# Optimization experiments

Measured on AMD Instinct MI355X. Metric: run time of the kernel, lower is better.

The kernel has to match this reference:

```python
import jax, jax.numpy as jnp
import numpy as np

N_NODES = 100000
N_EDGES = 1600000
D_IN = 64
D_HID = 128
BN_EPS = 1e-5


def setup_inputs() -> dict:
    key = jax.random.key(0)
    ks = jax.random.split(key, 8)
    x = jax.random.normal(ks[0], (N_NODES, D_IN), dtype=jnp.float32)
    edge_index = jax.random.randint(ks[1], (2, N_EDGES), 0, N_NODES, dtype=jnp.int64)
    # MLP params (Linear stores W as [out, in]; we keep [in, out] for x @ W)
    s1 = 1.0 / np.sqrt(D_IN)
    s2 = 1.0 / np.sqrt(D_HID)
    W1 = jax.random.uniform(ks[2], (D_IN, D_HID), minval=-s1, maxval=s1, dtype=jnp.float32)
    b1 = jax.random.uniform(ks[3], (D_HID,), minval=-s1, maxval=s1, dtype=jnp.float32)
    W2 = jax.random.uniform(ks[4], (D_HID, D_HID), minval=-s2, maxval=s2, dtype=jnp.float32)
    b2 = jax.random.uniform(ks[5], (D_HID,), minval=-s2, maxval=s2, dtype=jnp.float32)
    gamma = jnp.ones((D_HID,), dtype=jnp.float32)
    beta = jnp.zeros((D_HID,), dtype=jnp.float32)
    return {"x": x, "edge_index": edge_index, "W1": W1, "b1": b1,
            "W2": W2, "b2": b2, "gamma": gamma, "beta": beta}


def reference(x, edge_index, W1, b1, W2, b2, gamma, beta):
    src, dst = edge_index[0], edge_index[1]
    # GIN sum aggregation: agg[i] = sum_{(j->i) in E} x[j]
    agg = jax.ops.segment_sum(x[src], dst, num_segments=N_NODES)
    h = x + agg  # eps = 0 (GINConv default)
    # 2-layer MLP with ReLU
    h = jax.nn.relu(h @ W1 + b1)
    h = h @ W2 + b2
    # outer ReLU
    h = jax.nn.relu(h)
    # BatchNorm1d (training mode: biased batch statistics over nodes)
    mean = jnp.mean(h, axis=0)
    var = jnp.var(h, axis=0)
    h = (h - mean) * jax.lax.rsqrt(var + BN_EPS) * gamma + beta
    return h
```

## Files before the change

### kernel.cpp

```cpp
#include <hip/hip_runtime.h>

#define N_NODES 100000
#define N_EDGES 1600000
#define D_IN 64
#define D_HID 128

typedef __attribute__((ext_vector_type(8))) _Float16 half8;
typedef __attribute__((ext_vector_type(4))) float f32x4;

__global__ __launch_bounds__(256) void k_hist(const int* __restrict__ dst,
                                              int* __restrict__ counts) {
    int e = blockIdx.x * 256 + threadIdx.x;
    atomicAdd(&counts[dst[e]], 1);
}

__global__ __launch_bounds__(256) void k_scan1(const int* __restrict__ counts,
                                               int* __restrict__ loc,
                                               int* __restrict__ bsum) {
    __shared__ int tmp[256];
    int t = threadIdx.x;
    int base = blockIdx.x * 1024 + t * 4;
    int v0 = (base + 0 < N_NODES) ? counts[base + 0] : 0;
    int v1 = (base + 1 < N_NODES) ? counts[base + 1] : 0;
    int v2 = (base + 2 < N_NODES) ? counts[base + 2] : 0;
    int v3 = (base + 3 < N_NODES) ? counts[base + 3] : 0;
    tmp[t] = v0 + v1 + v2 + v3;
    __syncthreads();
    for (int off = 1; off < 256; off <<= 1) {
        int val = tmp[t];
        int add = (t >= off) ? tmp[t - off] : 0;
        __syncthreads();
        tmp[t] = val + add;
        __syncthreads();
    }
    int excl = t ? tmp[t - 1] : 0;
    if (base + 0 < N_NODES) loc[base + 0] = excl;
    if (base + 1 < N_NODES) loc[base + 1] = excl + v0;
    if (base + 2 < N_NODES) loc[base + 2] = excl + v0 + v1;
    if (base + 3 < N_NODES) loc[base + 3] = excl + v0 + v1 + v2;
    if (t == 255) bsum[blockIdx.x] = tmp[255];
}

__global__ void k_scan2(const int* __restrict__ bsum, int* __restrict__ bpref) {
    __shared__ int tmp[128];
    int t = threadIdx.x;
    tmp[t] = (t < 98) ? bsum[t] : 0;
    __syncthreads();
    for (int off = 1; off < 128; off <<= 1) {
        int val = tmp[t];
        int add = (t >= off) ? tmp[t - off] : 0;
        __syncthreads();
        tmp[t] = val + add;
        __syncthreads();
    }
    bpref[t] = t ? tmp[t - 1] : 0;
}

__global__ __launch_bounds__(256) void k_scan3(const int* __restrict__ loc,
                                               const int* __restrict__ bpref,
                                               int* __restrict__ offs) {
    int i = blockIdx.x * 256 + threadIdx.x;
    if (i < N_NODES) offs[i] = loc[i] + bpref[i >> 10];
}

__global__ __launch_bounds__(256) void k_fill(const int* __restrict__ src,
                                              const int* __restrict__ dst,
                                              int* __restrict__ offs,
                                              int* __restrict__ srcs) {
    int e = blockIdx.x * 256 + threadIdx.x;
    int p = atomicAdd(&offs[dst[e]], 1);
    srcs[p] = src[e];
}

__global__ __launch_bounds__(256) void k_gather(const float* __restrict__ x,
                                                const int* __restrict__ offs_end,
                                                const int* __restrict__ counts,
                                                const int* __restrict__ srcs,
                                                _Float16* __restrict__ aggh) {
    int wid = (blockIdx.x * 256 + threadIdx.x) >> 6;
    int lane = threadIdx.x & 63;
    int end = offs_end[wid];
    int beg = end - counts[wid];
    float sum = x[(size_t)wid * 64 + lane];
    int e = beg;
    for (; e + 4 <= end; e += 4) {
        int s0 = srcs[e], s1 = srcs[e + 1], s2 = srcs[e + 2], s3 = srcs[e + 3];
        float a0 = x[(size_t)s0 * 64 + lane];
        float a1 = x[(size_t)s1 * 64 + lane];
        float a2 = x[(size_t)s2 * 64 + lane];
        float a3 = x[(size_t)s3 * 64 + lane];
        sum += a0 + a1 + a2 + a3;
    }
    for (; e < end; ++e) sum += x[(size_t)srcs[e] * 64 + lane];
    aggh[(size_t)wid * 64 + lane] = (_Float16)sum;
}

__global__ __launch_bounds__(256) void k_pack(const float* __restrict__ W1,
                                              const float* __restrict__ W2,
                                              _Float16* __restrict__ W1p,
                                              _Float16* __restrict__ W2p) {
    int t = blockIdx.x * 256 + threadIdx.x;
    if (t < 1024) {
        int l = t & 63;
        int row = ((t >> 9) & 1) * 32 + (l >> 4) * 8;
        int col = ((t >> 6) & 7) * 16 + (l & 15);
#pragma unroll
        for (int i = 0; i < 8; ++i)
            W1p[t * 8 + i] = (_Float16)W1[(row + i) * 128 + col];
    } else {
        int s = t - 1024;
        int l = s & 63;
        int row = (s >> 9) * 32 + (l >> 4) * 8;
        int col = ((s >> 6) & 7) * 16 + (l & 15);
#pragma unroll
        for (int i = 0; i < 8; ++i)
            W2p[s * 8 + i] = (_Float16)W2[(row + i) * 128 + col];
    }
}

__global__ __launch_bounds__(256) void k_gemm1(const _Float16* __restrict__ A,
                                               const _Float16* __restrict__ Wp,
                                               const float* __restrict__ bias,
                                               _Float16* __restrict__ H) {
    int lane = threadIdx.x & 63, wv = threadIdx.x >> 6;
    int row0 = blockIdx.x * 64 + wv * 16;
    int ar = row0 + (lane & 15);
    if (ar > N_NODES - 1) ar = N_NODES - 1;
    int ac = (lane >> 4) * 8;
    half8 a0 = *(const half8*)&A[(size_t)ar * 64 + ac];
    half8 a1 = *(const half8*)&A[(size_t)ar * 64 + 32 + ac];
    f32x4 acc[8];
#pragma unroll
    for (int ct = 0; ct < 8; ++ct) {
        half8 w0 = *(const half8*)&Wp[(size_t)(ct * 64 + lane) * 8];
        half8 w1 = *(const half8*)&Wp[(size_t)(512 + ct * 64 + lane) * 8];
        f32x4 c = {0.f, 0.f, 0.f, 0.f};
        c = __builtin_amdgcn_mfma_f32_16x16x32_f16(a0, w0, c, 0, 0, 0);
        c = __builtin_amdgcn_mfma_f32_16x16x32_f16(a1, w1, c, 0, 0, 0);
        acc[ct] = c;
    }
    int g = lane >> 4, cl = lane & 15;
#pragma unroll
    for (int ct = 0; ct < 8; ++ct) {
        int col = ct * 16 + cl;
        float b = bias[col];
#pragma unroll
        for (int r = 0; r < 4; ++r) {
            int row = row0 + g * 4 + r;
            if (row < N_NODES) {
                float v = fmaxf(acc[ct][r] + b, 0.f);
                H[(size_t)row * 128 + col] = (_Float16)v;
            }
        }
    }
}

__global__ __launch_bounds__(256) void k_gemm2(const _Float16* __restrict__ A,
                                               const _Float16* __restrict__ Wp,
                                               const float* __restrict__ bias,
                                               float* __restrict__ OUT,
                                               float* __restrict__ stats) {
    __shared__ float sred[4][256];
    int lane = threadIdx.x & 63, wv = threadIdx.x >> 6;
    int row0 = blockIdx.x * 64 + wv * 16;
    int ar = row0 + (lane & 15);
    if (ar > N_NODES - 1) ar = N_NODES - 1;
    int ac = (lane >> 4) * 8;
    half8 a[4];
#pragma unroll
    for (int kt = 0; kt < 4; ++kt)
        a[kt] = *(const half8*)&A[(size_t)ar * 128 + kt * 32 + ac];
    int g = lane >> 4, cl = lane & 15;
#pragma unroll
    for (int ct = 0; ct < 8; ++ct) {
        f32x4 c = {0.f, 0.f, 0.f, 0.f};
#pragma unroll
        for (int kt = 0; kt < 4; ++kt) {
            half8 w = *(const half8*)&Wp[(size_t)((kt * 8 + ct) * 64 + lane) * 8];
            c = __builtin_amdgcn_mfma_f32_16x16x32_f16(a[kt], w, c, 0, 0, 0);
        }
        int col = ct * 16 + cl;
        float b = bias[col];
        float s = 0.f, q = 0.f;
#pragma unroll
        for (int r = 0; r < 4; ++r) {
            int row = row0 + g * 4 + r;
            float v = fmaxf(c[r] + b, 0.f);
            if (row < N_NODES) {
                OUT[(size_t)row * 128 + col] = v;
                s += v; q += v * v;
            }
        }
        s += __shfl_xor(s, 16); s += __shfl_xor(s, 32);
        q += __shfl_xor(q, 16); q += __shfl_xor(q, 32);
        if (g == 0) { sred[wv][col] = s; sred[wv][128 + col] = q; }
    }
    __syncthreads();
    int tid = threadIdx.x;
    float v = sred[0][tid] + sred[1][tid] + sred[2][tid] + sred[3][tid];
    unsafeAtomicAdd(&stats[tid], v);
}

__global__ void k_finalize(const float* __restrict__ stats,
                           const float* __restrict__ gamma,
                           const float* __restrict__ beta,
                           float* __restrict__ ss) {
    int c = threadIdx.x;
    float mean = stats[c] * (1.0f / N_NODES);
    float var = stats[128 + c] * (1.0f / N_NODES) - mean * mean;
    float scale = gamma[c] * rsqrtf(var + 1e-5f);
    ss[c] = scale;
    ss[128 + c] = beta[c] - mean * scale;
}

__global__ __launch_bounds__(256) void k_bn(float4* __restrict__ out,
                                            const float4* __restrict__ ss) {
    int stride = gridDim.x * 256;
    for (int f = blockIdx.x * 256 + threadIdx.x; f < N_NODES * 32; f += stride) {
        int c4 = f & 31;
        float4 sc = ss[c4];
        float4 sh = ss[32 + c4];
        float4 v = out[f];
        v.x = v.x * sc.x + sh.x;
        v.y = v.y * sc.y + sh.y;
        v.z = v.z * sc.z + sh.z;
        v.w = v.w * sc.w + sh.w;
        out[f] = v;
    }
}

extern "C" void kernel_launch(void* const* d_in, const int* in_sizes, int n_in,
                              void* d_out, int out_size, void* d_ws, size_t ws_size,
                              hipStream_t stream) {
    const float* x     = (const float*)d_in[0];
    const int*   ei    = (const int*)d_in[1];
    const float* W1    = (const float*)d_in[2];
    const float* b1    = (const float*)d_in[3];
    const float* W2    = (const float*)d_in[4];
    const float* b2    = (const float*)d_in[5];
    const float* gamma = (const float*)d_in[6];
    const float* beta  = (const float*)d_in[7];
    float* out = (float*)d_out;

    char* w = (char*)d_ws;
    _Float16* aggh = (_Float16*)w;  w += (size_t)N_NODES * D_IN * 2;
    _Float16* h1h  = (_Float16*)w;  w += (size_t)N_NODES * D_HID * 2;
    int* srcs      = (int*)w;       w += (size_t)N_EDGES * 4;
    int* counts    = (int*)w;       w += N_NODES * 4;
    int* loc       = (int*)w;       w += N_NODES * 4;
    int* offs      = (int*)w;       w += N_NODES * 4;
    int* bsum      = (int*)w;       w += 512;
    int* bpref     = (int*)w;       w += 512;
    float* stats   = (float*)w;     w += 1024;
    float* ss      = (float*)w;     w += 1024;
    _Float16* W1p  = (_Float16*)w;  w += 16384;
    _Float16* W2p  = (_Float16*)w;  w += 32768;

    const int* src = ei;
    const int* dst = ei + N_EDGES;

    (void)hipMemsetAsync(counts, 0, N_NODES * sizeof(int), stream);
    (void)hipMemsetAsync(stats, 0, 256 * sizeof(float), stream);

    k_pack <<<12, 256, 0, stream>>>(W1, W2, W1p, W2p);
    k_hist <<<N_EDGES / 256, 256, 0, stream>>>(dst, counts);
    k_scan1<<<98, 256, 0, stream>>>(counts, loc, bsum);
    k_scan2<<<1, 128, 0, stream>>>(bsum, bpref);
    k_scan3<<<(N_NODES + 255) / 256, 256, 0, stream>>>(loc, bpref, offs);
    k_fill <<<N_EDGES / 256, 256, 0, stream>>>(src, dst, offs, srcs);
    k_gather<<<N_NODES / 4, 256, 0, stream>>>(x, offs, counts, srcs, aggh);

    k_gemm1<<<(N_NODES + 63) / 64, 256, 0, stream>>>(aggh, W1p, b1, h1h);
    k_gemm2<<<(N_NODES + 63) / 64, 256, 0, stream>>>(h1h, W2p, b2, out, stats);
    k_finalize<<<1, 128, 0, stream>>>(stats, gamma, beta, ss);
    k_bn<<<2048, 256, 0, stream>>>((float4*)out, (const float4*)ss);
}
```

Before: 447.5 us.

## Replace atomic CSR build with two-level bucketed sort and fp16 gather

Builds the destination-sorted edge list with a two-pass radix-style partition: per-block bin histograms in shared memory, a single-block scan, a scatter into 512-node bins, then a per-bin counting sort staged through shared memory. This replaces global atomics on 100k counters and random scattered writes. Node features are pre-converted to fp16, and the gather reads half2 with two edges per wave half, which halves gather bandwidth at the cost of fp16 rounding of the inputs before summation. The offsets array now carries an end sentinel instead of counts.

Measured after the change: 383.5 us. 1.17x faster.

```diff
diff --git a/kernel.cpp b/kernel.cpp
--- a/kernel.cpp
+++ b/kernel.cpp
@@ -1,98 +1,169 @@
 #include <hip/hip_runtime.h>
+#include <hip/hip_fp16.h>
 
 #define N_NODES 100000
 #define N_EDGES 1600000
 #define D_IN 64
 #define D_HID 128
+#define NBINS 196
+#define NBLK 200
+#define EPB 8000
+#define FCAP 10240
 
 typedef __attribute__((ext_vector_type(8))) _Float16 half8;
 typedef __attribute__((ext_vector_type(4))) float f32x4;
 
-__global__ __launch_bounds__(256) void k_hist(const int* __restrict__ dst,
-                                              int* __restrict__ counts) {
-    int e = blockIdx.x * 256 + threadIdx.x;
-    atomicAdd(&counts[dst[e]], 1);
-}
-
-__global__ __launch_bounds__(256) void k_scan1(const int* __restrict__ counts,
-                                               int* __restrict__ loc,
-                                               int* __restrict__ bsum) {
-    __shared__ int tmp[256];
+__device__ inline float2 h2f(unsigned u) {
+    __half2 h = __builtin_bit_cast(__half2, u);
+    return __half22float2(h);
+}
+__device__ inline unsigned f2h(float a, float b) {
+    __half2 h = __floats2half2_rn(a, b);
+    return __builtin_bit_cast(unsigned, h);
+}
+
+__global__ __launch_bounds__(256) void k_xhalf(const float4* __restrict__ x4,
+                                               uint2* __restrict__ xh2) {
+    int i = blockIdx.x * 256 + threadIdx.x;
+    float4 v = x4[i];
+    uint2 o;
+    o.x = f2h(v.x, v.y);
+    o.y = f2h(v.z, v.w);
+    xh2[i] = o;
+}
+
+__global__ __launch_bounds__(256) void k_pcount(const int* __restrict__ dst,
+                                                int* __restrict__ pbh) {
+    __shared__ int hist[NBINS];
+    int t = threadIdx.x, b = blockIdx.x;
+    if (t < NBINS) hist[t] = 0;
+    __syncthreads();
+    for (int i = t; i < EPB; i += 256)
+        atomicAdd(&hist[dst[b * EPB + i] >> 9], 1);
+    __syncthreads();
+    if (t < NBINS) pbh[t * NBLK + b] = hist[t];
+}
+
+__global__ void k_pscan(const int* __restrict__ pbh, int* __restrict__ pbo,
+                        int* __restrict__ binstart, int* __restrict__ offs) {
+    __shared__ int part[256];
+    const int TOT = NBINS * NBLK;
     int t = threadIdx.x;
-    int base = blockIdx.x * 1024 + t * 4;
-    int v0 = (base + 0 < N_NODES) ? counts[base + 0] : 0;
-    int v1 = (base + 1 < N_NODES) ? counts[base + 1] : 0;
-    int v2 = (base + 2 < N_NODES) ? counts[base + 2] : 0;
-    int v3 = (base + 3 < N_NODES) ? counts[base + 3] : 0;
-    tmp[t] = v0 + v1 + v2 + v3;
+    int lo = t * 154, hi = lo + 154 < TOT ? lo + 154 : TOT;
+    int s = 0;
+    for (int i = lo; i < hi; ++i) s += pbh[i];
+    part[t] = s;
     __syncthreads();
     for (int off = 1; off < 256; off <<= 1) {
-        int val = tmp[t];
-        int add = (t >= off) ? tmp[t - off] : 0;
+        int val = part[t];
+        int add = (t >= off) ? part[t - off] : 0;
         __syncthreads();
-        tmp[t] = val + add;
+        part[t] = val + add;
         __syncthreads();
     }
-    int excl = t ? tmp[t - 1] : 0;
-    if (base + 0 < N_NODES) loc[base + 0] = excl;
-    if (base + 1 < N_NODES) loc[base + 1] = excl + v0;
-    if (base + 2 < N_NODES) loc[base + 2] = excl + v0 + v1;
-    if (base + 3 < N_NODES) loc[base + 3] = excl + v0 + v1 + v2;
-    if (t == 255) bsum[blockIdx.x] = tmp[255];
-}
-
-__global__ void k_scan2(const int* __restrict__ bsum, int* __restrict__ bpref) {
-    __shared__ int tmp[128];
-    int t = threadIdx.x;
-    tmp[t] = (t < 98) ? bsum[t] : 0;
-    __syncthreads();
-    for (int off = 1; off < 128; off <<= 1) {
-        int val = tmp[t];
-        int add = (t >= off) ? tmp[t - off] : 0;
+    int run = t ? part[t - 1] : 0;
+    for (int i = lo; i < hi; ++i) {
+        int v = pbh[i];
+        pbo[i] = run;
+        if ((i % NBLK) == 0) binstart[i / NBLK] = run;
+        run += v;
+    }
+    if (t == 0) { binstart[NBINS] = N_EDGES; offs[N_NODES] = N_EDGES; }
+}
+
+__global__ __launch_bounds__(256) void k_pscatter(const int* __restrict__ src,
+                                                  const int* __restrict__ dst,
+                                                  const int* __restrict__ pbo,
+                                                  unsigned* __restrict__ packed) {
+    __shared__ int cur[NBINS];
+    int t = threadIdx.x, b = blockIdx.x;
+    if (t < NBINS) cur[t] = pbo[t * NBLK + b];
+    __syncthreads();
+    for (int i = t; i < EPB; i += 256) {
+        int e = b * EPB + i;
+        int d = dst[e];
+        int bin = d >> 9;
+        int p = atomicAdd(&cur[bin], 1);
+        packed[p] = ((unsigned)(d & 511) << 17) | (unsigned)src[e];
+    }
+}
+
+__global__ __launch_bounds__(256) void k_fsort(const unsigned* __restrict__ packed,
+                                               const int* __restrict__ binstart,
+                                               int* __restrict__ offs,
+                                               int* __restrict__ srcs) {
+    __shared__ int nh[512];
+    __shared__ int cur[512];
+    __shared__ int part[256];
+    __shared__ int stage[FCAP];
+    int t = threadIdx.x, bin = blockIdx.x;
+    int base = binstart[bin];
+    int n = binstart[bin + 1] - base;
+    nh[t] = 0; nh[t + 256] = 0;
+    __syncthreads();
+    for (int i = t; i < n; i += 256)
+        atomicAdd(&nh[packed[base + i] >> 17], 1);
+    __syncthreads();
+    int a0 = nh[2 * t], a1 = nh[2 * t + 1];
+    part[t] = a0 + a1;
+    __syncthreads();
+    for (int off = 1; off < 256; off <<= 1) {
+        int val = part[t];
+        int add = (t >= off) ? part[t - off] : 0;
         __syncthreads();
-        tmp[t] = val + add;
+        part[t] = val + add;
         __syncthreads();
     }
-    bpref[t] = t ? tmp[t - 1] : 0;
-}
-
-__global__ __launch_bounds__(256) void k_scan3(const int* __restrict__ loc,
-                                               const int* __restrict__ bpref,
-                                               int* __restrict__ offs) {
-    int i = blockIdx.x * 256 + threadIdx.x;
-    if (i < N_NODES) offs[i] = loc[i] + bpref[i >> 10];
-}
-
-__global__ __launch_bounds__(256) void k_fill(const int* __restrict__ src,
-                                              const int* __restrict__ dst,
-                                              int* __restrict__ offs,
-                                              int* __restrict__ srcs) {
-    int e = blockIdx.x * 256 + threadIdx.x;
-    int p = atomicAdd(&offs[dst[e]], 1);
-    srcs[p] = src[e];
-}
-
-__global__ __launch_bounds__(256) void k_gather(const float* __restrict__ x,
-                                                const int* __restrict__ offs_end,
-                                                const int* __restrict__ counts,
+    int excl = t ? part[t - 1] : 0;
+    cur[2 * t] = excl;
+    cur[2 * t + 1] = excl + a0;
+    int node0 = bin * 512 + 2 * t;
+    if (node0 < N_NODES) offs[node0] = base + excl;
+    if (node0 + 1 < N_NODES) offs[node0 + 1] = base + excl + a0;
+    __syncthreads();
+    for (int i = t; i < n; i += 256) {
+        unsigned u = packed[base + i];
+        int dl = u >> 17;
+        int s = u & 0x1FFFF;
+        int p = atomicAdd(&cur[dl], 1);
+        if (p < FCAP) stage[p] = s;
+        else srcs[base + p] = s;
+    }
+    __syncthreads();
+    int m = n < FCAP ? n : FCAP;
+    for (int i = t; i < m; i += 256) srcs[base + i] = stage[i];
+}
+
+__global__ __launch_bounds__(256) void k_gather(const unsigned* __restrict__ xh,
+                                                const int* __restrict__ offs,
                                                 const int* __restrict__ srcs,
-                                                _Float16* __restrict__ aggh) {
+                                                unsigned* __restrict__ aggh) {
     int wid = (blockIdx.x * 256 + threadIdx.x) >> 6;
     int lane = threadIdx.x & 63;
-    int end = offs_end[wid];
-    int beg = end - counts[wid];
-    float sum = x[(size_t)wid * 64 + lane];
+    int half = lane >> 5, c = lane & 31;
+    int beg = offs[wid], end = offs[wid + 1];
+    float2 sum;
+    if (half == 0) sum = h2f(xh[(size_t)wid * 32 + c]);
+    else sum = make_float2(0.f, 0.f);
     int e = beg;
     for (; e + 4 <= end; e += 4) {
-        int s0 = srcs[e], s1 = srcs[e + 1], s2 = srcs[e + 2], s3 = srcs[e + 3];
-        float a0 = x[(size_t)s0 * 64 + lane];
-        float a1 = x[(size_t)s1 * 64 + lane];
-        float a2 = x[(size_t)s2 * 64 + lane];
-        float a3 = x[(size_t)s3 * 64 + lane];
-        sum += a0 + a1 + a2 + a3;
-    }
-    for (; e < end; ++e) sum += x[(size_t)srcs[e] * 64 + lane];
-    aggh[(size_t)wid * 64 + lane] = (_Float16)sum;
+        int i0 = e + half, i1 = e + 2 + half;
+        int s0 = srcs[i0], s1 = srcs[i1];
+        float2 v0 = h2f(xh[(size_t)s0 * 32 + c]);
+        float2 v1 = h2f(xh[(size_t)s1 * 32 + c]);
+        sum.x += v0.x + v1.x;
+        sum.y += v0.y + v1.y;
+    }
+    for (; e < end; e += 2) {
+        int idx = e + half;
+        if (idx < end) {
+            float2 v = h2f(xh[(size_t)srcs[idx] * 32 + c]);
+            sum.x += v.x; sum.y += v.y;
+        }
+    }
+    sum.x += __shfl_xor(sum.x, 32);
+    sum.y += __shfl_xor(sum.y, 32);
+    if (half == 0) aggh[(size_t)wid * 32 + c] = f2h(sum.x, sum.y);
 }
 
 __global__ __launch_bounds__(256) void k_pack(const float* __restrict__ W1,
@@ -243,14 +314,15 @@
     float* out = (float*)d_out;
 
     char* w = (char*)d_ws;
-    _Float16* aggh = (_Float16*)w;  w += (size_t)N_NODES * D_IN * 2;
+    unsigned* xh   = (unsigned*)w;  w += (size_t)N_NODES * 32 * 4;
+    unsigned* aggh = (unsigned*)w;  w += (size_t)N_NODES * 32 * 4;
     _Float16* h1h  = (_Float16*)w;  w += (size_t)N_NODES * D_HID * 2;
+    unsigned* packed = (unsigned*)w; w += (size_t)N_EDGES * 4;
     int* srcs      = (int*)w;       w += (size_t)N_EDGES * 4;
-    int* counts    = (int*)w;       w += N_NODES * 4;
-    int* loc       = (int*)w;       w += N_NODES * 4;
-    int* offs      = (int*)w;       w += N_NODES * 4;
-    int* bsum      = (int*)w;       w += 512;
-    int* bpref     = (int*)w;       w += 512;
+    int* offs      = (int*)w;       w += (N_NODES + 1) * 4;
+    int* pbh       = (int*)w;       w += NBINS * NBLK * 4;
+    int* pbo       = (int*)w;       w += NBINS * NBLK * 4;
+    int* binstart  = (int*)w;       w += (NBINS + 1) * 4;
     float* stats   = (float*)w;     w += 1024;
     float* ss      = (float*)w;     w += 1024;
     _Float16* W1p  = (_Float16*)w;  w += 16384;
@@ -259,18 +331,17 @@
     const int* src = ei;
     const int* dst = ei + N_EDGES;
 
-    (void)hipMemsetAsync(counts, 0, N_NODES * sizeof(int), stream);
     (void)hipMemsetAsync(stats, 0, 256 * sizeof(float), stream);
 
-    k_pack <<<12, 256, 0, stream>>>(W1, W2, W1p, W2p);
-    k_hist <<<N_EDGES / 256, 256, 0, stream>>>(dst, counts);
-    k_scan1<<<98, 256, 0, stream>>>(counts, loc, bsum);
-    k_scan2<<<1, 128, 0, stream>>>(bsum, bpref);
-    k_scan3<<<(N_NODES + 255) / 256, 256, 0, stream>>>(loc, bpref, offs);
-    k_fill <<<N_EDGES / 256, 256, 0, stream>>>(src, dst, offs, srcs);
-    k_gather<<<N_NODES / 4, 256, 0, stream>>>(x, offs, counts, srcs, aggh);
-
-    k_gemm1<<<(N_NODES + 63) / 64, 256, 0, stream>>>(aggh, W1p, b1, h1h);
+    k_pack    <<<12, 256, 0, stream>>>(W1, W2, W1p, W2p);
+    k_xhalf   <<<N_NODES * 64 / 4 / 256, 256, 0, stream>>>((const float4*)x, (uint2*)xh);
+    k_pcount  <<<NBLK, 256, 0, stream>>>(dst, pbh);
+    k_pscan   <<<1, 256, 0, stream>>>(pbh, pbo, binstart, offs);
+    k_pscatter<<<NBLK, 256, 0, stream>>>(src, dst, pbo, packed);
+    k_fsort   <<<NBINS, 256, 0, stream>>>(packed, binstart, offs, srcs);
+    k_gather  <<<N_NODES / 4, 256, 0, stream>>>(xh, offs, srcs, aggh);
+
+    k_gemm1<<<(N_NODES + 63) / 64, 256, 0, stream>>>((const _Float16*)aggh, W1p, b1, h1h);
     k_gemm2<<<(N_NODES + 63) / 64, 256, 0, stream>>>(h1h, W2p, b2, out, stats);
     k_finalize<<<1, 128, 0, stream>>>(stats, gamma, beta, ss);
     k_bn<<<2048, 256, 0, stream>>>((float4*)out, (const float4*)ss);
```
